# Kernel tuning notes

Measured on AMD Instinct MI355X. Metric: run time of the kernel, lower is better.

Reference implementation:

```python
import jax, jax.numpy as jnp
import numpy as np

N, D, H = 4096, 1024, 8
DH = D // H
EPS = 1e-5


def layer_norm(x, g, b):
    mu = jnp.mean(x, axis=-1, keepdims=True)
    var = jnp.mean(jnp.square(x - mu), axis=-1, keepdims=True)
    return (x - mu) * jax.lax.rsqrt(var + EPS) * g + b


def setup_inputs() -> dict:
    key = jax.random.key(0)
    ks = jax.random.split(key, 12)
    s = 0.02
    inp = {
        "x": jax.random.normal(ks[0], (N, D), dtype=jnp.float32),
        "adj": (jax.random.uniform(ks[1], (N, N)) < 0.01).astype(jnp.float32),
        "Wq": jax.random.normal(ks[2], (D, D), dtype=jnp.float32) * s,
        "Wk": jax.random.normal(ks[3], (D, D), dtype=jnp.float32) * s,
        "Wv": jax.random.normal(ks[4], (D, D), dtype=jnp.float32) * s,
        "Wo_w": jax.random.normal(ks[5], (D, D), dtype=jnp.float32) * s,
        "Wo_b": jnp.zeros((D,), dtype=jnp.float32),
        "adj_bias": jnp.full((H,), 1.0, dtype=jnp.float32),
        "ln1_g": jnp.ones((D,), dtype=jnp.float32),
        "ln1_b": jnp.zeros((D,), dtype=jnp.float32),
        "ffn_ln_g": jnp.ones((D,), dtype=jnp.float32),
        "ffn_ln_b": jnp.zeros((D,), dtype=jnp.float32),
        "ffn_w1": jax.random.normal(ks[6], (D, 2 * D), dtype=jnp.float32) * s,
        "ffn_b1": jnp.zeros((2 * D,), dtype=jnp.float32),
        "ffn_w2": jax.random.normal(ks[7], (2 * D, D), dtype=jnp.float32) * s,
        "ffn_b2": jnp.zeros((D,), dtype=jnp.float32),
    }
    return inp


def reference(x, adj, Wq, Wk, Wv, Wo_w, Wo_b, adj_bias, ln1_g, ln1_b,
              ffn_ln_g, ffn_ln_b, ffn_w1, ffn_b1, ffn_w2, ffn_b2):
    scale = DH ** -0.5
    Q = (x @ Wq).reshape(N, H, DH)
    K = (x @ Wk).reshape(N, H, DH)
    V = (x @ Wv).reshape(N, H, DH)
    # attn[i,h,j] = <Q_i, K_j> * scale + beta_h * adj[i,j]
    attn = jnp.einsum('bhd,nhd->bhn', Q, K) * scale
    attn = attn + adj_bias[None, :, None] * adj[:, None, :]
    attn = jax.nn.softmax(attn, axis=-1)  # dropout in eval mode -> identity
    out = jnp.einsum('bhn,nhd->bhd', attn, V).reshape(N, D)
    out = out @ Wo_w + Wo_b
    h = layer_norm(x + out, ln1_g, ln1_b)
    f = layer_norm(h, ffn_ln_g, ffn_ln_b)
    f = jax.nn.gelu(f @ ffn_w1 + ffn_b1, approximate=False) @ ffn_w2 + ffn_b2
    return h + f
```

## Files before the change

### kernel.cpp

```cpp
#include <hip/hip_runtime.h>
#include <hip/hip_bf16.h>
#include <cstdint>
#include <cstddef>

typedef __hip_bfloat16 bf16;
typedef __attribute__((ext_vector_type(8))) short short8;
typedef __attribute__((ext_vector_type(4))) short short4v;
typedef __attribute__((ext_vector_type(4))) float floatx4;
typedef unsigned long long u64;

#define DEVI static __device__ __forceinline__

DEVI void load_lds16(const void* g, void* l) {
  __builtin_amdgcn_global_load_lds((const __attribute__((address_space(1))) unsigned int*)g,
                                   (__attribute__((address_space(3))) unsigned int*)l, 16, 0, 0);
}
DEVI short8 ld8(const bf16* p) { return *(const short8*)p; }
DEVI floatx4 mfma16(short8 a, short8 b, floatx4 c) {
  return __builtin_amdgcn_mfma_f32_16x16x32_bf16(a, b, c, 0, 0, 0);
}
DEVI short bfb(float f) { bf16 h = __float2bfloat16(f); return __builtin_bit_cast(short, h); }
DEVI float fbf(short s) { bf16 h = __builtin_bit_cast(bf16, s); return __bfloat162float(h); }

DEVI short4v sm4(floatx4 s, uint32_t u, int bp, float scale2, float beta2) {
  short4v r;
  float p0 = __builtin_amdgcn_exp2f(fmaf(s[0], scale2, ((u >> (bp + 0)) & 1) ? beta2 : 0.f));
  float p1 = __builtin_amdgcn_exp2f(fmaf(s[1], scale2, ((u >> (bp + 1)) & 1) ? beta2 : 0.f));
  float p2 = __builtin_amdgcn_exp2f(fmaf(s[2], scale2, ((u >> (bp + 2)) & 1) ? beta2 : 0.f));
  float p3 = __builtin_amdgcn_exp2f(fmaf(s[3], scale2, ((u >> (bp + 3)) & 1) ? beta2 : 0.f));
  r.x = bfb(p0); r.y = bfb(p1); r.z = bfb(p2); r.w = bfb(p3);
  return r;
}

DEVI void tr_tile(const float* in, bf16* out, int R, int C, int bx, int by) {
  __shared__ float t[32][33];
  int c0 = bx * 32, r0 = by * 32;
  int tx = threadIdx.x & 31, ty = threadIdx.x >> 5;
#pragma unroll
  for (int i = 0; i < 32; i += 8) t[ty + i][tx] = in[(size_t)(r0 + ty + i) * C + c0 + tx];
  __syncthreads();
#pragma unroll
  for (int i = 0; i < 32; i += 8)
    out[(size_t)(c0 + ty + i) * R + r0 + tx] = __float2bfloat16(t[tx][ty + i]);
}

__global__ __launch_bounds__(256)
void prep_all(const float* __restrict__ x, bf16* __restrict__ xb,
              const float* __restrict__ adj, u64* __restrict__ bits,
              const float* Wq, const float* Wk, const float* Wv, const float* Wo,
              const float* W1, const float* W2,
              bf16* Wqkvt, bf16* Wot, bf16* W1t, bf16* W2t) {
  int id = blockIdx.x;
  if (id < 4096) {
    const int row = id, tid = threadIdx.x;
    const int wave = tid >> 6, lane = tid & 63;
    float4 v = ((const float4*)(x + (size_t)row * 1024))[tid];
    bf16* o = xb + (size_t)row * 1024 + tid * 4;
    o[0] = __float2bfloat16(v.x); o[1] = __float2bfloat16(v.y);
    o[2] = __float2bfloat16(v.z); o[3] = __float2bfloat16(v.w);
    const float* arow = adj + (size_t)row * 4096;
#pragma unroll
    for (int it = 0; it < 16; it++) {
      int col = it * 256 + tid;
      u64 m = __ballot(arow[col] != 0.f);
      if (lane == 0) bits[(size_t)row * 64 + it * 4 + wave] = m;
    }
  } else if (id < 8192) {
    int q = id - 4096, w = q >> 10, t = q & 1023;
    const float* in = w == 0 ? Wq : w == 1 ? Wk : w == 2 ? Wv : Wo;
    bf16* out = w == 0 ? Wqkvt : w == 1 ? Wqkvt + 1024ull * 1024
              : w == 2 ? Wqkvt + 2048ull * 1024 : Wot;
    tr_tile(in, out, 1024, 1024, t & 31, t >> 5);
  } else if (id < 10240) {
    int t = id - 8192;
    tr_tile(W1, W1t, 1024, 2048, t & 63, t >> 6);
  } else {
    int t = id - 10240;
    tr_tile(W2, W2t, 2048, 1024, t & 31, t >> 5);
  }
}

__global__ __launch_bounds__(256)
void tr_bf16t(const bf16* __restrict__ in, bf16* __restrict__ out, int inLd) {
  __shared__ bf16 t[32][33];
  int c0 = blockIdx.x * 32, r0 = blockIdx.y * 32;
  int tx = threadIdx.x, ty = threadIdx.y;
#pragma unroll
  for (int i = 0; i < 32; i += 8) t[ty + i][tx] = in[(size_t)(r0 + ty + i) * inLd + c0 + tx];
  __syncthreads();
#pragma unroll
  for (int i = 0; i < 32; i += 8)
    out[(size_t)(c0 + ty + i) * 4096 + r0 + tx] = t[tx][ty + i];
}

template <int MODE, int BN>
__global__ __launch_bounds__(256, 3)
void gemm_bt(const bf16* __restrict__ A, const bf16* __restrict__ Bt,
             const float* __restrict__ bias, const float* __restrict__ resid,
             float* __restrict__ outF, bf16* __restrict__ outB,
             int M, int Nn, int K) {
  constexpr int NI = BN / 32;
  __shared__ alignas(16) bf16 As[3][128 * 32];
  __shared__ alignas(16) bf16 Bs[3][BN * 32];
  const int tid = threadIdx.x;
  const int wave = tid >> 6, lane = tid & 63;
  const int gx = gridDim.x, nwg = gx * gridDim.y;
  const int lin = blockIdx.x + gx * blockIdx.y;
  const int swz = (lin & 7) * (nwg >> 3) + (lin >> 3);
  const int m0 = (swz / gx) * 128, n0 = (swz % gx) * BN;
  const int wr = (wave >> 1) * 64, wc = (wave & 1) * (BN / 2);
  const int l15 = lane & 15, qq = lane >> 4;
  const int lr = lane >> 2, l4 = lane & 3;
  const int T = K >> 5;

  floatx4 acc[4][NI];
#pragma unroll
  for (int i = 0; i < 4; i++)
#pragma unroll
    for (int j = 0; j < NI; j++) acc[i][j] = (floatx4)0.f;

  const bf16* gA0 = A + (size_t)(m0 + wave * 16 + lr) * K + l4 * 8;
  const bf16* gA1 = gA0 + (size_t)64 * K;
  const bf16* gB0 = Bt + (size_t)(n0 + wave * 16 + lr) * K + l4 * 8;
  const bf16* gB1 = gB0 + (size_t)64 * K;
  const int lo = wave * 16 * 32;

  auto stage = [&](int t, int buf) {
    int kt = t * 32;
    load_lds16(gA0 + kt, &As[buf][lo]);
    load_lds16(gA1 + kt, &As[buf][64 * 32 + lo]);
    load_lds16(gB0 + kt, &Bs[buf][lo]);
    if (BN == 128) load_lds16(gB1 + kt, &Bs[buf][64 * 32 + lo]);
  };
  stage(0, 0);
  stage(1, 1);

  int bc = 0;
  for (int t = 0; t < T; ++t) {
    if (t < T - 1) {
      if constexpr (BN == 128)
        asm volatile("s_waitcnt vmcnt(4) lgkmcnt(0)" ::: "memory");
      else
        asm volatile("s_waitcnt vmcnt(3) lgkmcnt(0)" ::: "memory");
    } else {
      asm volatile("s_waitcnt vmcnt(0) lgkmcnt(0)" ::: "memory");
    }
    __builtin_amdgcn_s_barrier();
    if (t + 2 < T) { int bs = bc == 0 ? 2 : bc - 1; stage(t + 2, bs); }

    short8 af[4], bfr[NI];
#pragma unroll
    for (int mi = 0; mi < 4; mi++) af[mi] = ld8(&As[bc][(wr + mi * 16 + l15) * 32 + qq * 8]);
#pragma unroll
    for (int ni = 0; ni < NI; ni++) bfr[ni] = ld8(&Bs[bc][(wc + ni * 16 + l15) * 32 + qq * 8]);
#pragma unroll
    for (int mi = 0; mi < 4; mi++)
#pragma unroll
      for (int ni = 0; ni < NI; ni++)
        acc[mi][ni] = mfma16(af[mi], bfr[ni], acc[mi][ni]);
    bc = bc == 2 ? 0 : bc + 1;
  }

#pragma unroll
  for (int mi = 0; mi < 4; mi++) {
    int row = m0 + wr + mi * 16 + qq * 4;
#pragma unroll
    for (int ni = 0; ni < NI; ni++) {
      int col = n0 + wc + ni * 16 + l15;
      float bv = (MODE >= 1) ? bias[col] : 0.f;
#pragma unroll
      for (int r = 0; r < 4; r++) {
        float v = acc[mi][ni][r] + bv;
        size_t off = (size_t)(row + r) * Nn + col;
        if (MODE == 0) {
          outB[off] = __float2bfloat16(v);
        } else if (MODE == 2) {
          outB[off] = __float2bfloat16(0.5f * v * (1.f + erff(v * 0.70710678118654752f)));
        } else if (MODE == 1) {
          outF[off] = v;
        } else {
          outF[off] = v + resid[off];
        }
      }
    }
  }
}

__global__ __launch_bounds__(256, 2)
void attn_kernel(const bf16* __restrict__ QKV, const bf16* __restrict__ Vt,
                 const u64* __restrict__ adjbits, const float* __restrict__ adj_bias,
                 bf16* __restrict__ AOpart, float* __restrict__ lpart) {
  __shared__ alignas(16) bf16 Kf[2][16 * 512];
  __shared__ alignas(16) bf16 Vf[2][16 * 512];
  const int L = blockIdx.x;
  const int xr = L & 7, rest = L >> 3;
  const int qi = rest & 31, chi = rest >> 5;
  const int c = xr + 8 * chi;
  const int h = c >> 1, split = c & 1;
  const int q0 = qi * 128;
  const int k0 = split * 2048;
  const int tid = threadIdx.x, wave = tid >> 6, lane = tid & 63;
  const int l15 = lane & 15, qq = lane >> 4;
  const float log2e = 1.4426950408889634f;
  const float beta2 = adj_bias[h] * log2e;
  const float scale2 = 0.08838834764831845f * log2e;

  short8 qf[2][4];
#pragma unroll
  for (int mi = 0; mi < 2; mi++)
#pragma unroll
    for (int kk = 0; kk < 4; kk++)
      qf[mi][kk] = ld8(&QKV[(size_t)(q0 + wave * 32 + mi * 16 + l15) * 3072 +
                            h * 128 + kk * 32 + qq * 8]);

  floatx4 o[2][8];
#pragma unroll
  for (int mi = 0; mi < 2; mi++)
#pragma unroll
    for (int d = 0; d < 8; d++) o[mi][d] = (floatx4)0.f;
  floatx4 o8[2] = {(floatx4)0.f, (floatx4)0.f};
  short8 ones;
#pragma unroll
  for (int i = 0; i < 8; i++) ones[i] = (short)0x3F80;

  const size_t abase = (size_t)(q0 + wave * 32 + l15) * 64 + split * 32;
  const int kperm = ((l15 >> 2) * 8) + (l15 & 3);

  auto stage = [&](int t, int buf) {
    const int kt = k0 + t * 64;
#pragma unroll
    for (int i = 0; i < 4; i++) {
      int fi = wave * 4 + i;
      int ni = fi >> 2, kk = fi & 3;
      int krow = kt + (ni >> 1) * 32 + (ni & 1) * 4 + kperm;
      load_lds16(&QKV[(size_t)krow * 3072 + 1024 + h * 128 + kk * 32 + qq * 8],
                 (char*)Kf[buf] + fi * 1024);
      int d = fi >> 1, k2 = fi & 1;
      load_lds16(&Vt[(size_t)(h * 128 + d * 16 + l15) * 4096 + kt + k2 * 32 + qq * 8],
                 (char*)Vf[buf] + fi * 1024);
    }
  };

  stage(0, 0);
  u64 a0c = adjbits[abase];
  u64 a1c = adjbits[abase + 1024];

  const int bp = qq * 8;

  for (int t = 0; t < 32; t++) {
    __syncthreads();
    if (t < 31) stage(t + 1, (t + 1) & 1);
    u64 a0n = 0, a1n = 0;
    if (t < 31) { a0n = adjbits[abase + t + 1]; a1n = adjbits[abase + 1024 + t + 1]; }

    const bf16* Kc = Kf[t & 1];
    const char* Vcb = (const char*)Vf[t & 1];
    const uint32_t w0lo = (uint32_t)a0c, w0hi = (uint32_t)(a0c >> 32);
    const uint32_t w1lo = (uint32_t)a1c, w1hi = (uint32_t)(a1c >> 32);

    short8 k0r[8], v0r[8];
#pragma unroll
    for (int kk = 0; kk < 4; kk++) {
      k0r[kk]     = ld8(&Kc[(0 * 4 + kk) * 512 + lane * 8]);
      k0r[4 + kk] = ld8(&Kc[(1 * 4 + kk) * 512 + lane * 8]);
    }
#pragma unroll
    for (int d = 0; d < 8; d++)
      v0r[d] = ld8((const bf16*)(Vcb + (d * 2 + 0) * 1024 + qq * 256 + l15 * 16));

    floatx4 s00 = (floatx4)0.f, s10 = (floatx4)0.f;
    floatx4 s01 = (floatx4)0.f, s11 = (floatx4)0.f;
    __builtin_amdgcn_s_setprio(1);
#pragma unroll
    for (int kk = 0; kk < 4; kk++) {
      s00 = mfma16(k0r[kk], qf[0][kk], s00);
      s10 = mfma16(k0r[kk], qf[1][kk], s10);
    }
#pragma unroll
    for (int kk = 0; kk < 4; kk++) {
      s01 = mfma16(k0r[4 + kk], qf[0][kk], s01);
      s11 = mfma16(k0r[4 + kk], qf[1][kk], s11);
    }
    __builtin_amdgcn_s_setprio(0);

    short8 k1r[8], v1r[8];
#pragma unroll
    for (int kk = 0; kk < 4; kk++) {
      k1r[kk]     = ld8(&Kc[(2 * 4 + kk) * 512 + lane * 8]);
      k1r[4 + kk] = ld8(&Kc[(3 * 4 + kk) * 512 + lane * 8]);
    }
#pragma unroll
    for (int d = 0; d < 8; d++)
      v1r[d] = ld8((const bf16*)(Vcb + (d * 2 + 1) * 1024 + qq * 256 + l15 * 16));

    floatx4 u00 = (floatx4)0.f, u10 = (floatx4)0.f;
    floatx4 u01 = (floatx4)0.f, u11 = (floatx4)0.f;
    __builtin_amdgcn_s_setprio(1);
#pragma unroll
    for (int kk = 0; kk < 4; kk++) {
      u00 = mfma16(k1r[kk], qf[0][kk], u00);
      u10 = mfma16(k1r[kk], qf[1][kk], u10);
    }
#pragma unroll
    for (int kk = 0; kk < 4; kk++) {
      u01 = mfma16(k1r[4 + kk], qf[0][kk], u01);
      u11 = mfma16(k1r[4 + kk], qf[1][kk], u11);
    }
    __builtin_amdgcn_s_setprio(0);

    short8 pa0, pa1;
    {
      short4v a = sm4(s00, w0lo, bp, scale2, beta2);
      short4v b = sm4(s01, w0lo >> 4, bp, scale2, beta2);
      pa0[0] = a.x; pa0[1] = a.y; pa0[2] = a.z; pa0[3] = a.w;
      pa0[4] = b.x; pa0[5] = b.y; pa0[6] = b.z; pa0[7] = b.w;
      a = sm4(s10, w1lo, bp, scale2, beta2);
      b = sm4(s11, w1lo >> 4, bp, scale2, beta2);
      pa1[0] = a.x; pa1[1] = a.y; pa1[2] = a.z; pa1[3] = a.w;
      pa1[4] = b.x; pa1[5] = b.y; pa1[6] = b.z; pa1[7] = b.w;
    }
    __builtin_amdgcn_s_setprio(1);
#pragma unroll
    for (int d = 0; d < 8; d++) {
      o[0][d] = mfma16(pa0, v0r[d], o[0][d]);
      o[1][d] = mfma16(pa1, v0r[d], o[1][d]);
    }
    o8[0] = mfma16(pa0, ones, o8[0]);
    o8[1] = mfma16(pa1, ones, o8[1]);
    __builtin_amdgcn_s_setprio(0);

    short8 pb0, pb1;
    {
      short4v a = sm4(u00, w0hi, bp, scale2, beta2);
      short4v b = sm4(u01, w0hi >> 4, bp, scale2, beta2);
      pb0[0] = a.x; pb0[1] = a.y; pb0[2] = a.z; pb0[3] = a.w;
      pb0[4] = b.x; pb0[5] = b.y; pb0[6] = b.z; pb0[7] = b.w;
      a = sm4(u10, w1hi, bp, scale2, beta2);
      b = sm4(u11, w1hi >> 4, bp, scale2, beta2);
      pb1[0] = a.x; pb1[1] = a.y; pb1[2] = a.z; pb1[3] = a.w;
      pb1[4] = b.x; pb1[5] = b.y; pb1[6] = b.z; pb1[7] = b.w;
    }
    __builtin_amdgcn_s_setprio(1);
#pragma unroll
    for (int d = 0; d < 8; d++) {
      o[0][d] = mfma16(pb0, v1r[d], o[0][d]);
      o[1][d] = mfma16(pb1, v1r[d], o[1][d]);
    }
    o8[0] = mfma16(pb0, ones, o8[0]);
    o8[1] = mfma16(pb1, ones, o8[1]);
    __builtin_amdgcn_s_setprio(0);

    a0c = a0n; a1c = a1n;
  }

#pragma unroll
  for (int mi = 0; mi < 2; mi++) {
    if (l15 == 0) {
#pragma unroll
      for (int r = 0; r < 4; r++)
        lpart[((size_t)split * 4096 + q0 + wave * 32 + mi * 16 + qq * 4 + r) * 8 + h] =
            o8[mi][r];
    }
#pragma unroll
    for (int r = 0; r < 4; r++) {
      int grow = q0 + wave * 32 + mi * 16 + qq * 4 + r;
      bf16* dst = AOpart + ((size_t)split * 4096 + grow) * 1024 + h * 128;
#pragma unroll
      for (int d = 0; d < 8; d++) dst[d * 16 + l15] = __float2bfloat16(o[mi][d][r]);
    }
  }
}

__global__ __launch_bounds__(256)
void attn_norm(const bf16* __restrict__ AOpart, const float* __restrict__ lpart,
               bf16* __restrict__ AO) {
  int row = blockIdx.x, tid = threadIdx.x;
  int h = tid >> 5;
  float ls = 0.f;
#pragma unroll
  for (int s = 0; s < 2; s++) ls += lpart[((size_t)s * 4096 + row) * 8 + h];
  float a0 = 0.f, a1 = 0.f, a2 = 0.f, a3 = 0.f;
#pragma unroll
  for (int s = 0; s < 2; s++) {
    short4v v = *(const short4v*)&AOpart[((size_t)s * 4096 + row) * 1024 + tid * 4];
    a0 += fbf(v.x); a1 += fbf(v.y); a2 += fbf(v.z); a3 += fbf(v.w);
  }
  float inv = 1.f / ls;
  bf16* op = AO + (size_t)row * 1024 + tid * 4;
  op[0] = __float2bfloat16(a0 * inv);
  op[1] = __float2bfloat16(a1 * inv);
  op[2] = __float2bfloat16(a2 * inv);
  op[3] = __float2bfloat16(a3 * inv);
}

DEVI void block_sum2(float& a, float& b, float* red) {
#pragma unroll
  for (int o = 1; o < 64; o <<= 1) { a += __shfl_xor(a, o, 64); b += __shfl_xor(b, o, 64); }
  int wv = threadIdx.x >> 6;
  if ((threadIdx.x & 63) == 0) { red[wv] = a; red[4 + wv] = b; }
  __syncthreads();
  a = red[0] + red[1] + red[2] + red[3];
  b = red[4] + red[5] + red[6] + red[7];
  __syncthreads();
}

__global__ __launch_bounds__(256)
void ln2_kernel(const float* __restrict__ x, const float* __restrict__ ao,
                const float* __restrict__ g1, const float* __restrict__ b1,
                const float* __restrict__ g2, const float* __restrict__ b2,
                float* __restrict__ hout, bf16* __restrict__ fln) {
  __shared__ float red[8];
  const int row = blockIdx.x, tid = threadIdx.x;
  float4 xv = ((const float4*)(x + (size_t)row * 1024))[tid];
  float4 av = ((const float4*)(ao + (size_t)row * 1024))[tid];
  float s0 = xv.x + av.x, s1 = xv.y + av.y, s2 = xv.z + av.z, s3 = xv.w + av.w;
  float sum = s0 + s1 + s2 + s3;
  float ssq = s0 * s0 + s1 * s1 + s2 * s2 + s3 * s3;
  block_sum2(sum, ssq, red);
  float mu = sum * (1.f / 1024.f);
  float rs = rsqrtf(ssq * (1.f / 1024.f) - mu * mu + 1e-5f);
  float4 gv = ((const float4*)g1)[tid], bv = ((const float4*)b1)[tid];
  float h0 = (s0 - mu) * rs * gv.x + bv.x;
  float h1 = (s1 - mu) * rs * gv.y + bv.y;
  float h2 = (s2 - mu) * rs * gv.z + bv.z;
  float h3 = (s3 - mu) * rs * gv.w + bv.w;
  float4 hv; hv.x = h0; hv.y = h1; hv.z = h2; hv.w = h3;
  ((float4*)(hout + (size_t)row * 1024))[tid] = hv;
  float sum2 = h0 + h1 + h2 + h3;
  float ssq2 = h0 * h0 + h1 * h1 + h2 * h2 + h3 * h3;
  block_sum2(sum2, ssq2, red);
  float mu2 = sum2 * (1.f / 1024.f);
  float rs2 = rsqrtf(ssq2 * (1.f / 1024.f) - mu2 * mu2 + 1e-5f);
  float4 g2v = ((const float4*)g2)[tid], b2v = ((const float4*)b2)[tid];
  bf16* op = fln + (size_t)row * 1024 + tid * 4;
  op[0] = __float2bfloat16((h0 - mu2) * rs2 * g2v.x + b2v.x);
  op[1] = __float2bfloat16((h1 - mu2) * rs2 * g2v.y + b2v.y);
  op[2] = __float2bfloat16((h2 - mu2) * rs2 * g2v.z + b2v.z);
  op[3] = __float2bfloat16((h3 - mu2) * rs2 * g2v.w + b2v.w);
}

extern "C" void kernel_launch(void* const* d_in, const int* in_sizes, int n_in,
                              void* d_out, int out_size, void* d_ws, size_t ws_size,
                              hipStream_t stream) {
  const float* x    = (const float*)d_in[0];
  const float* adj  = (const float*)d_in[1];
  const float* Wq   = (const float*)d_in[2];
  const float* Wk   = (const float*)d_in[3];
  const float* Wv   = (const float*)d_in[4];
  const float* Wo   = (const float*)d_in[5];
  const float* Wob  = (const float*)d_in[6];
  const float* adjb = (const float*)d_in[7];
  const float* g1   = (const float*)d_in[8];
  const float* b1   = (const float*)d_in[9];
  const float* g2   = (const float*)d_in[10];
  const float* b2   = (const float*)d_in[11];
  const float* W1   = (const float*)d_in[12];
  const float* fb1  = (const float*)d_in[13];
  const float* W2   = (const float*)d_in[14];
  const float* fb2  = (const float*)d_in[15];
  float* out = (float*)d_out;

  char* w = (char*)d_ws;
  size_t off = 0;
  auto take = [&](size_t bytes) {
    char* p = w + off;
    off += (bytes + 255) & ~(size_t)255;
    return p;
  };
  bf16* xb    = (bf16*)take(4096ull * 1024 * 2);
  bf16* Wqkvt = (bf16*)take(3072ull * 1024 * 2);
  bf16* Wot   = (bf16*)take(1024ull * 1024 * 2);
  bf16* W1t   = (bf16*)take(2048ull * 1024 * 2);
  bf16* W2t   = (bf16*)take(1024ull * 2048 * 2);
  bf16* QKV   = (bf16*)take(4096ull * 3072 * 2);
  bf16* Vt    = (bf16*)take(1024ull * 4096 * 2);
  bf16* AO    = (bf16*)take(4096ull * 1024 * 2);
  u64*  adjbits = (u64*)take(4096ull * 64 * 8);
  float* lpart  = (float*)take(4ull * 4096 * 8 * 4);
  char* big = take(32ull << 20);
  bf16*  AOpart = (bf16*)big;
  float* WoP    = (float*)big;
  float* H   = (float*)take(4096ull * 1024 * 4);
  bf16*  FLN = (bf16*)take(4096ull * 1024 * 2);
  bf16*  G   = (bf16*)take(4096ull * 2048 * 2);

  dim3 tb(32, 8);
  prep_all<<<12288, 256, 0, stream>>>(x, xb, adj, adjbits, Wq, Wk, Wv, Wo, W1, W2,
                                      Wqkvt, Wot, W1t, W2t);
  gemm_bt<0, 128><<<dim3(24, 32), 256, 0, stream>>>(xb, Wqkvt, nullptr, nullptr,
                                                    nullptr, QKV, 4096, 3072, 1024);
  tr_bf16t<<<dim3(32, 128), tb, 0, stream>>>(QKV + 2048, Vt, 3072);
  attn_kernel<<<512, 256, 0, stream>>>(QKV, Vt, adjbits, adjb, AOpart, lpart);
  attn_norm<<<4096, 256, 0, stream>>>(AOpart, lpart, AO);
  gemm_bt<1, 64><<<dim3(16, 32), 256, 0, stream>>>(AO, Wot, Wob, nullptr,
                                                   WoP, nullptr, 4096, 1024, 1024);
  ln2_kernel<<<4096, 256, 0, stream>>>(x, WoP, g1, b1, g2, b2, H, FLN);
  gemm_bt<2, 128><<<dim3(16, 32), 256, 0, stream>>>(FLN, W1t, fb1, nullptr,
                                                    nullptr, G, 4096, 2048, 1024);
  gemm_bt<3, 64><<<dim3(16, 32), 256, 0, stream>>>(G, W2t, fb2, H,
                                                   out, nullptr, 4096, 1024, 2048);
}
```

Baseline: 403.7 us.

## Fuse attention split-merge normalization into the output projection GEMM A-load

Removes the separate attn_norm kernel and the AO intermediate buffer. The new gemm_ao kernel reads both bf16 attention partials plus the row sums, adds and normalizes them in registers, and writes the merged A tile to LDS. B is still staged asynchronously across a 3-buffer pipeline. This saves a kernel launch and a round trip of the AO tensor through memory. The cost is twice the A global loads inside the GEMM plus conversion ALU work on the critical path, and WoP now reuses the QKV buffer.

```diff
diff --git a/kernel.cpp b/kernel.cpp
--- a/kernel.cpp
+++ b/kernel.cpp
@@ -176,12 +176,122 @@
           outB[off] = __float2bfloat16(v);
         } else if (MODE == 2) {
           outB[off] = __float2bfloat16(0.5f * v * (1.f + erff(v * 0.70710678118654752f)));
-        } else if (MODE == 1) {
-          outF[off] = v;
         } else {
           outF[off] = v + resid[off];
         }
       }
+    }
+  }
+}
+
+__global__ __launch_bounds__(256, 2)
+void gemm_ao(const bf16* __restrict__ AOpart, const float* __restrict__ lpart,
+             const bf16* __restrict__ Bt, const float* __restrict__ bias,
+             float* __restrict__ outF) {
+  constexpr int BN = 64, NI = 2, K = 1024, Nn = 1024, T = 32;
+  __shared__ alignas(16) bf16 As[3][128 * 32];
+  __shared__ alignas(16) bf16 Bs[3][BN * 32];
+  const int tid = threadIdx.x;
+  const int wave = tid >> 6, lane = tid & 63;
+  const int gx = gridDim.x, nwg = gx * gridDim.y;
+  const int lin = blockIdx.x + gx * blockIdx.y;
+  const int swz = (lin & 7) * (nwg >> 3) + (lin >> 3);
+  const int m0 = (swz / gx) * 128, n0 = (swz % gx) * BN;
+  const int wr = (wave >> 1) * 64, wc = (wave & 1) * (BN / 2);
+  const int l15 = lane & 15, qq = lane >> 4;
+  const int lr = lane >> 2, l4 = lane & 3;
+  const int r0 = m0 + wave * 16 + lr;
+
+  floatx4 acc[4][NI];
+#pragma unroll
+  for (int i = 0; i < 4; i++)
+#pragma unroll
+    for (int j = 0; j < NI; j++) acc[i][j] = (floatx4)0.f;
+
+  float inv0[8], inv1[8];
+#pragma unroll
+  for (int rr = 0; rr < 2; rr++) {
+    int row = r0 + rr * 64;
+    float4 a = *(const float4*)&lpart[(size_t)row * 8];
+    float4 b = *(const float4*)&lpart[(size_t)row * 8 + 4];
+    float4 c = *(const float4*)&lpart[(size_t)(4096 + row) * 8];
+    float4 d = *(const float4*)&lpart[(size_t)(4096 + row) * 8 + 4];
+    float* iv = rr == 0 ? inv0 : inv1;
+    iv[0] = 1.f / (a.x + c.x); iv[1] = 1.f / (a.y + c.y);
+    iv[2] = 1.f / (a.z + c.z); iv[3] = 1.f / (a.w + c.w);
+    iv[4] = 1.f / (b.x + d.x); iv[5] = 1.f / (b.y + d.y);
+    iv[6] = 1.f / (b.z + d.z); iv[7] = 1.f / (b.w + d.w);
+  }
+
+  const bf16* gB0 = Bt + (size_t)(n0 + wave * 16 + lr) * K + l4 * 8;
+  const int lo = wave * 16 * 32;
+
+  auto Aload = [&](int t, short8& x0, short8& x1, short8& y0, short8& y1) {
+    int kt = t * 32 + l4 * 8;
+    x0 = ld8(&AOpart[(size_t)r0 * 1024 + kt]);
+    x1 = ld8(&AOpart[(size_t)(4096 + r0) * 1024 + kt]);
+    y0 = ld8(&AOpart[(size_t)(r0 + 64) * 1024 + kt]);
+    y1 = ld8(&AOpart[(size_t)(4096 + r0 + 64) * 1024 + kt]);
+  };
+  auto Aconv = [&](int t, int buf, short8 x0, short8 x1, short8 y0, short8 y1) {
+    float iva = inv0[t >> 2], ivb = inv1[t >> 2];
+    short8 o0, o1;
+#pragma unroll
+    for (int j = 0; j < 8; j++) {
+      o0[j] = bfb((fbf(x0[j]) + fbf(x1[j])) * iva);
+      o1[j] = bfb((fbf(y0[j]) + fbf(y1[j])) * ivb);
+    }
+    *(short8*)&As[buf][lo + lane * 8] = o0;
+    *(short8*)&As[buf][64 * 32 + lo + lane * 8] = o1;
+  };
+  auto Bstage = [&](int t, int buf) { load_lds16(gB0 + t * 32, &Bs[buf][lo]); };
+
+  short8 ax0, ax1, ay0, ay1;
+  Aload(0, ax0, ax1, ay0, ay1);
+  Aconv(0, 0, ax0, ax1, ay0, ay1);
+  Bstage(0, 0);
+  Aload(1, ax0, ax1, ay0, ay1);
+  Bstage(1, 1);
+
+  int bc = 0;
+  for (int t = 0; t < T; ++t) {
+    if (t < T - 1) {
+      asm volatile("s_waitcnt vmcnt(5) lgkmcnt(0)" ::: "memory");
+    } else {
+      asm volatile("s_waitcnt vmcnt(0) lgkmcnt(0)" ::: "memory");
+    }
+    __builtin_amdgcn_s_barrier();
+    if (t + 1 < T) {
+      short8 nx0 = ax0, nx1 = ax1, ny0 = ay0, ny1 = ay1;
+      if (t + 2 < T) Aload(t + 2, ax0, ax1, ay0, ay1);
+      int bn = bc == 0 ? 1 : (bc == 1 ? 2 : 0);
+      Aconv(t + 1, bn, nx0, nx1, ny0, ny1);
+      if (t + 2 < T) { int bs = bc == 0 ? 2 : bc - 1; Bstage(t + 2, bs); }
+    }
+
+    short8 af[4], bfr[NI];
+#pragma unroll
+    for (int mi = 0; mi < 4; mi++) af[mi] = ld8(&As[bc][(wr + mi * 16 + l15) * 32 + qq * 8]);
+#pragma unroll
+    for (int ni = 0; ni < NI; ni++) bfr[ni] = ld8(&Bs[bc][(wc + ni * 16 + l15) * 32 + qq * 8]);
+#pragma unroll
+    for (int mi = 0; mi < 4; mi++)
+#pragma unroll
+      for (int ni = 0; ni < NI; ni++)
+        acc[mi][ni] = mfma16(af[mi], bfr[ni], acc[mi][ni]);
+    bc = bc == 2 ? 0 : bc + 1;
+  }
+
+#pragma unroll
+  for (int mi = 0; mi < 4; mi++) {
+    int row = m0 + wr + mi * 16 + qq * 4;
+#pragma unroll
+    for (int ni = 0; ni < NI; ni++) {
+      int col = n0 + wc + ni * 16 + l15;
+      float bv = bias[col];
+#pragma unroll
+      for (int r = 0; r < 4; r++)
+        outF[(size_t)(row + r) * Nn + col] = acc[mi][ni][r] + bv;
     }
   }
 }
@@ -369,28 +479,6 @@
       for (int d = 0; d < 8; d++) dst[d * 16 + l15] = __float2bfloat16(o[mi][d][r]);
     }
   }
-}
-
-__global__ __launch_bounds__(256)
-void attn_norm(const bf16* __restrict__ AOpart, const float* __restrict__ lpart,
-               bf16* __restrict__ AO) {
-  int row = blockIdx.x, tid = threadIdx.x;
-  int h = tid >> 5;
-  float ls = 0.f;
-#pragma unroll
-  for (int s = 0; s < 2; s++) ls += lpart[((size_t)s * 4096 + row) * 8 + h];
-  float a0 = 0.f, a1 = 0.f, a2 = 0.f, a3 = 0.f;
-#pragma unroll
-  for (int s = 0; s < 2; s++) {
-    short4v v = *(const short4v*)&AOpart[((size_t)s * 4096 + row) * 1024 + tid * 4];
-    a0 += fbf(v.x); a1 += fbf(v.y); a2 += fbf(v.z); a3 += fbf(v.w);
-  }
-  float inv = 1.f / ls;
-  bf16* op = AO + (size_t)row * 1024 + tid * 4;
-  op[0] = __float2bfloat16(a0 * inv);
-  op[1] = __float2bfloat16(a1 * inv);
-  op[2] = __float2bfloat16(a2 * inv);
-  op[3] = __float2bfloat16(a3 * inv);
 }
 
 DEVI void block_sum2(float& a, float& b, float* red) {
@@ -474,12 +562,10 @@
   bf16* W2t   = (bf16*)take(1024ull * 2048 * 2);
   bf16* QKV   = (bf16*)take(4096ull * 3072 * 2);
   bf16* Vt    = (bf16*)take(1024ull * 4096 * 2);
-  bf16* AO    = (bf16*)take(4096ull * 1024 * 2);
   u64*  adjbits = (u64*)take(4096ull * 64 * 8);
   float* lpart  = (float*)take(4ull * 4096 * 8 * 4);
-  char* big = take(32ull << 20);
-  bf16*  AOpart = (bf16*)big;
-  float* WoP    = (float*)big;
+  bf16* AOpart = (bf16*)take(32ull << 20);
+  float* WoP = (float*)QKV;
   float* H   = (float*)take(4096ull * 1024 * 4);
   bf16*  FLN = (bf16*)take(4096ull * 1024 * 2);
   bf16*  G   = (bf16*)take(4096ull * 2048 * 2);
@@ -491,9 +577,7 @@
                                                     nullptr, QKV, 4096, 3072, 1024);
   tr_bf16t<<<dim3(32, 128), tb, 0, stream>>>(QKV + 2048, Vt, 3072);
   attn_kernel<<<512, 256, 0, stream>>>(QKV, Vt, adjbits, adjb, AOpart, lpart);
-  attn_norm<<<4096, 256, 0, stream>>>(AOpart, lpart, AO);
-  gemm_bt<1, 64><<<dim3(16, 32), 256, 0, stream>>>(AO, Wot, Wob, nullptr,
-                                                   WoP, nullptr, 4096, 1024, 1024);
+  gemm_ao<<<dim3(16, 32), 256, 0, stream>>>(AOpart, lpart, Wot, Wob, WoP);
   ln2_kernel<<<4096, 256, 0, stream>>>(x, WoP, g1, b1, g2, b2, H, FLN);
   gemm_bt<2, 128><<<dim3(16, 32), 256, 0, stream>>>(FLN, W1t, fb1, nullptr,
                                                     nullptr, G, 4096, 2048, 1024);
```

Result: no change. 408.9 us (+1.3%).
